# Kernel optimization log

Hardware: AMD Instinct MI355X
Metric: run time of the kernel (lower is better)

The kernel has to match this reference:

```python
import jax, jax.numpy as jnp
import numpy as np

D_MODEL = 1024
NUM_HEADS = 16
HEAD_DIM = D_MODEL // NUM_HEADS


def setup_inputs() -> dict:
    key = jax.random.key(0)
    ks = jax.random.split(key, 7)
    B, S = 2, 2048
    scale = 1.0 / np.sqrt(D_MODEL)
    inp = {
        "input": jax.random.normal(ks[0], (B, S, D_MODEL), dtype=jnp.float32),
        "W_q": jax.random.normal(ks[1], (D_MODEL, D_MODEL), dtype=jnp.float32) * scale,
        "b_q": jax.random.normal(ks[2], (D_MODEL,), dtype=jnp.float32) * 0.01,
        "W_k": jax.random.normal(ks[3], (D_MODEL, D_MODEL), dtype=jnp.float32) * scale,
        "b_k": jax.random.normal(ks[4], (D_MODEL,), dtype=jnp.float32) * 0.01,
        "W_v": jax.random.normal(ks[5], (D_MODEL, D_MODEL), dtype=jnp.float32) * scale,
        "b_v": jax.random.normal(ks[6], (D_MODEL,), dtype=jnp.float32) * 0.01,
    }
    return inp


def reference(input, W_q, b_q, W_k, b_k, W_v, b_v):
    B, S, _ = input.shape
    # QKV projections (torch nn.Linear: x @ W^T + b); split heads -> [B,H,S,Dh]
    def proj(W, b):
        y = jnp.einsum('bsd,ed->bse', input, W) + b
        return y.reshape(B, S, NUM_HEADS, HEAD_DIM).transpose(0, 2, 1, 3)

    Q = proj(W_q, b_q)
    K = proj(W_k, b_k)
    V = proj(W_v, b_v)

    scores = jnp.einsum('bhqd,bhkd->bhqk', Q, K) / jnp.sqrt(
        jnp.asarray(HEAD_DIM, dtype=input.dtype))
    attention_weights = jax.nn.softmax(scores, axis=-1)  # [B,H,S,S]
    out = jnp.einsum('bhqk,bhkd->bhqd', attention_weights, V)
    out = out.transpose(0, 2, 1, 3).reshape(B, S, D_MODEL)
    return out, attention_weights
```

## Files before the change

kernel.cpp:

```cpp
#include <hip/hip_runtime.h>
#include <stdint.h>

#define S_LEN   2048
#define D_MODEL 1024
#define N_HEADS 16
#define HEAD_D  64
#define BATCH   2
#define M_TOT   (BATCH * S_LEN)

typedef __attribute__((ext_vector_type(8))) short s8v;
typedef __attribute__((ext_vector_type(4))) float f4v;
typedef __attribute__((ext_vector_type(4))) unsigned short u4v;

__device__ __forceinline__ float bf2f(unsigned short u) {
    union { unsigned int i; float f; } c; c.i = ((unsigned int)u) << 16; return c.f;
}
__device__ __forceinline__ unsigned short f2bf(float f) {
    union { float f; unsigned int i; } c; c.f = f;
    unsigned int u = c.i + 0x7FFFu + ((c.i >> 16) & 1u);
    return (unsigned short)(u >> 16);
}
__device__ __forceinline__ unsigned int pk2bf(float lo, float hi) {
    return (unsigned int)f2bf(lo) | ((unsigned int)f2bf(hi) << 16);
}
__device__ __forceinline__ float hw_exp2(float x) { return __builtin_amdgcn_exp2f(x); }

#define GLD16(gp, lp) __builtin_amdgcn_global_load_lds(                      \
    (const __attribute__((address_space(1))) void*)(const void*)(gp),        \
    (__attribute__((address_space(3))) void*)(void*)(lp), 16, 0, 0)

#define BAR_LGKM() asm volatile("s_waitcnt lgkmcnt(0)\n\ts_barrier" ::: "memory")

#define EXP_SCALE 0.1803368801111204f

__global__ __launch_bounds__(256) void cvt_bf16(const float* __restrict__ src,
                                                unsigned short* __restrict__ dst, int n) {
    int i = (blockIdx.x * 256 + threadIdx.x) * 4;
    int stride = gridDim.x * 1024;
    for (; i < n; i += stride) {
        float4 v = *(const float4*)(src + i);
        u4v o;
        o[0] = f2bf(v.x); o[1] = f2bf(v.y); o[2] = f2bf(v.z); o[3] = f2bf(v.w);
        *(u4v*)(dst + i) = o;
    }
}

__global__ __launch_bounds__(256) void qkv_gemm(
    const unsigned short* __restrict__ X,
    const unsigned short* __restrict__ Wq, const unsigned short* __restrict__ Wk,
    const unsigned short* __restrict__ Wv,
    const float* __restrict__ bq, const float* __restrict__ bk, const float* __restrict__ bv,
    unsigned short* __restrict__ q_ws, unsigned short* __restrict__ k_ws,
    unsigned short* __restrict__ vt_ws) {
    __shared__ unsigned short sA[128 * 32];
    __shared__ unsigned short sB[128 * 32];

    const int z = blockIdx.z;
    const unsigned short* Wm = (z == 0) ? Wq : ((z == 1) ? Wk : Wv);
    const float* bm = (z == 0) ? bq : ((z == 1) ? bk : bv);
    const int m0 = blockIdx.x * 128, n0 = blockIdx.y * 128;
    const int t = threadIdx.x;
    const int lane = t & 63, w = t >> 6;
    const int fr = lane & 15, g = lane >> 4;
    const int wr = w >> 1, wc = w & 1;

    f4v acc[4][4];
#pragma unroll
    for (int i = 0; i < 4; ++i)
#pragma unroll
        for (int j = 0; j < 4; ++j) acc[i][j] = (f4v){0.f, 0.f, 0.f, 0.f};

    const int rowL = t >> 2;
    const int colL = (t & 3) * 8;
    const unsigned short* gA = X + (size_t)(m0 + rowL) * D_MODEL + colL;
    const unsigned short* gB = Wm + (size_t)(n0 + rowL) * D_MODEL + colL;

    for (int kb = 0; kb < 32; ++kb) {
        const int k0 = kb * 32;
        GLD16(gA + k0,                 sA + w * 512);
        GLD16(gA + 64 * D_MODEL + k0,  sA + 2048 + w * 512);
        GLD16(gB + k0,                 sB + w * 512);
        GLD16(gB + 64 * D_MODEL + k0,  sB + 2048 + w * 512);
        __syncthreads();

        s8v af[4], bfv[4];
#pragma unroll
        for (int i = 0; i < 4; ++i)
            af[i] = *(const s8v*)(sA + (wr * 64 + i * 16 + fr) * 32 + g * 8);
#pragma unroll
        for (int j = 0; j < 4; ++j)
            bfv[j] = *(const s8v*)(sB + (wc * 64 + j * 16 + fr) * 32 + g * 8);
#pragma unroll
        for (int i = 0; i < 4; ++i)
#pragma unroll
            for (int j = 0; j < 4; ++j)
                acc[i][j] = __builtin_amdgcn_mfma_f32_16x16x32_bf16(af[i], bfv[j], acc[i][j], 0, 0, 0);
        __syncthreads();
    }

    const int e_base = n0 + wc * 64;
    const int m_base = m0 + wr * 64;
    if (z < 2) {
        unsigned short* dst = (z == 0) ? q_ws : k_ws;
#pragma unroll
        for (int i = 0; i < 4; ++i) {
#pragma unroll
            for (int j = 0; j < 4; ++j) {
                const int e = e_base + j * 16 + fr;
                const int h = e >> 6, dh = e & 63;
                const float bias = bm[e];
                const int mr = m_base + i * 16 + g * 4;
                const int b_ = mr >> 11, srow = mr & 2047;
                const size_t base = (((size_t)(b_ * N_HEADS + h) * S_LEN + srow) << 6) + dh;
#pragma unroll
                for (int r = 0; r < 4; ++r)
                    dst[base + ((size_t)r << 6)] = f2bf(acc[i][j][r] + bias);
            }
        }
    } else {
#pragma unroll
        for (int i = 0; i < 4; ++i) {
#pragma unroll
            for (int j = 0; j < 4; ++j) {
                const int e = e_base + j * 16 + fr;
                const int h = e >> 6, dh = e & 63;
                const float bias = bm[e];
                const int mr = m_base + i * 16 + g * 4;
                const int b_ = mr >> 11, srow = mr & 2047;
                u4v pk;
#pragma unroll
                for (int r = 0; r < 4; ++r) pk[r] = f2bf(acc[i][j][r] + bias);
                *(u4v*)(vt_ws + ((size_t)(b_ * N_HEADS + h) * HEAD_D + dh) * S_LEN + srow) = pk;
            }
        }
    }
}

__global__ __launch_bounds__(256, 4) void attn_fused6(
    const unsigned short* __restrict__ q_ws, const unsigned short* __restrict__ k_ws,
    const unsigned short* __restrict__ vt_ws,
    float* __restrict__ out, float* __restrict__ wts) {
    __shared__ __align__(16) char SM[40960];

    const int t = threadIdx.x, lane = t & 63, w = t >> 6;
    const int fr = lane & 15, g = lane >> 4;
    const int blk = blockIdx.x;
    const int bh = (blk & 7) * 4 + (blk >> 8);
    const int qt = (blk >> 3) & 31;

    const unsigned short* Qp = q_ws + ((size_t)bh * S_LEN + qt * 64 + w * 16) * HEAD_D;
    const unsigned short* Kp = k_ws + (size_t)bh * S_LEN * HEAD_D;
    const unsigned short* Vt = vt_ws + (size_t)bh * HEAD_D * S_LEN;

    const s8v qa0 = *(const s8v*)(Qp + fr * HEAD_D + g * 8);
    const s8v qa1 = *(const s8v*)(Qp + fr * HEAD_D + 32 + g * 8);

    auto stageK64 = [&](int c, char* dst) {
#pragma unroll
        for (int j = 0; j < 2; ++j) {
            const int d = t * 16 + j * 4096;
            const int row = d >> 7, cb = (d >> 4) & 7;
            GLD16(Kp + (size_t)(c * 64 + row) * HEAD_D + ((cb ^ (row & 7)) << 3),
                  dst + w * 1024 + j * 4096);
        }
    };
    auto stageV64 = [&](int c, char* dst) {
#pragma unroll
        for (int j = 0; j < 2; ++j) {
            const int d = t * 16 + j * 4096;
            const int row = d >> 7, cb = (d >> 4) & 7;
            GLD16(Vt + (size_t)row * S_LEN + c * 64 + ((cb ^ (row & 7)) << 3),
                  dst + w * 1024 + j * 4096);
        }
    };
    auto stageK128 = [&](int c, char* dst) {
#pragma unroll
        for (int j = 0; j < 4; ++j) {
            const int d = t * 16 + j * 4096;
            const int row = d >> 7, cb = (d >> 4) & 7;
            GLD16(Kp + (size_t)(c * 128 + row) * HEAD_D + ((cb ^ (row & 7)) << 3),
                  dst + w * 1024 + j * 4096);
        }
    };
    auto qk16 = [&](const char* kb, int st) -> f4v {
        const int row = st * 16 + fr, m = row & 7;
        const s8v ka0 = *(const s8v*)(kb + row * 128 + ((g ^ m) << 4));
        const s8v ka1 = *(const s8v*)(kb + row * 128 + (((4 + g) ^ m) << 4));
        f4v s = (f4v){0.f, 0.f, 0.f, 0.f};
        s = __builtin_amdgcn_mfma_f32_16x16x32_bf16(ka0, qa0, s, 0, 0, 0);
        s = __builtin_amdgcn_mfma_f32_16x16x32_bf16(ka1, qa1, s, 0, 0, 0);
        return s;
    };

    float rsum = 0.f;
    stageK128(0, SM);
    for (int c = 0; c < 16; ++c) {
        const int cur = c & 1;
        if (c < 15) stageK128(c + 1, SM + (cur ^ 1) * 16384);
        if (c < 15) asm volatile("s_waitcnt vmcnt(4)" ::: "memory");
        else        asm volatile("s_waitcnt vmcnt(0)" ::: "memory");
        asm volatile("s_barrier" ::: "memory");
        const char* kb = SM + cur * 16384;
#pragma unroll
        for (int st = 0; st < 8; ++st) {
            const f4v s = qk16(kb, st);
#pragma unroll
            for (int r = 0; r < 4; ++r) rsum += hw_exp2(s[r] * EXP_SCALE);
        }
        BAR_LGKM();
    }
    rsum += __shfl_xor(rsum, 16);
    rsum += __shfl_xor(rsum, 32);
    const float inv = 1.f / rsum;

    f4v acc[4];
#pragma unroll
    for (int i = 0; i < 4; ++i) acc[i] = (f4v){0.f, 0.f, 0.f, 0.f};
    unsigned short* PL = (unsigned short*)(SM + 32768 + w * 2048);
    const int swp = (fr & 7) << 4;
    float* wbase = wts + ((size_t)bh * S_LEN + qt * 64 + w * 16) * S_LEN;

    stageK64(0, SM); stageV64(0, SM + 16384);
    for (int c = 0; c < 32; ++c) {
        const int cur = c & 1;
        if (c < 31) { stageK64(c + 1, SM + (cur ^ 1) * 8192);
                      stageV64(c + 1, SM + 16384 + (cur ^ 1) * 8192); }
        if (c == 0)      asm volatile("s_waitcnt vmcnt(4)" ::: "memory");
        else if (c < 31) asm volatile("s_waitcnt vmcnt(8)" ::: "memory");
        else             asm volatile("s_waitcnt vmcnt(4)" ::: "memory");
        asm volatile("s_barrier" ::: "memory");

        const char* kb = SM + cur * 8192;
#pragma unroll
        for (int st = 0; st < 4; ++st) {
            const f4v s = qk16(kb, st);
            f4v p;
#pragma unroll
            for (int r = 0; r < 4; ++r) p[r] = hw_exp2(s[r] * EXP_SCALE) * inv;
            const int base = fr * 128 + st * 32 + g * 8;
            *(unsigned int*)((char*)PL + ((base)     ^ swp)) = pk2bf(p[0], p[1]);
            *(unsigned int*)((char*)PL + ((base + 4) ^ swp)) = pk2bf(p[2], p[3]);
        }

        {
            const int r0 = lane >> 4, cc = lane & 15;
#pragma unroll
            for (int i = 0; i < 4; ++i) {
                const int row = i * 4 + r0;
                const u4v pw = *(const u4v*)((const char*)PL +
                                             ((row * 128 + cc * 8) ^ ((row & 7) << 4)));
                f4v o;
#pragma unroll
                for (int e = 0; e < 4; ++e) o[e] = bf2f(pw[e]);
                __builtin_nontemporal_store(o,
                    (f4v*)(wbase + (size_t)row * S_LEN + c * 64 + cc * 4));
            }
        }

        const char* vl = SM + 16384 + cur * 8192;
#pragma unroll
        for (int ks = 0; ks < 2; ++ks) {
            const s8v pa = *(const s8v*)((const char*)PL +
                                         ((fr * 128 + ks * 64 + g * 16) ^ swp));
#pragma unroll
            for (int tt = 0; tt < 4; ++tt) {
                const int vrow = tt * 16 + fr;
                const s8v vv = *(const s8v*)(vl + vrow * 128 +
                                             (((ks * 4 + g) ^ (vrow & 7)) << 4));
                acc[tt] = __builtin_amdgcn_mfma_f32_16x16x32_bf16(pa, vv, acc[tt], 0, 0, 0);
            }
        }
        BAR_LGKM();
    }

    const int b_ = bh >> 4, h = bh & 15;
#pragma unroll
    for (int tt = 0; tt < 4; ++tt)
#pragma unroll
        for (int r = 0; r < 4; ++r)
            __builtin_nontemporal_store(acc[tt][r],
                &out[((size_t)b_ * S_LEN + qt * 64 + w * 16 + g * 4 + r) * D_MODEL +
                     h * HEAD_D + tt * 16 + fr]);
}

extern "C" void kernel_launch(void* const* d_in, const int* in_sizes, int n_in,
                              void* d_out, int out_size, void* d_ws, size_t ws_size,
                              hipStream_t stream) {
    const float* x  = (const float*)d_in[0];
    const float* Wq = (const float*)d_in[1];
    const float* bq = (const float*)d_in[2];
    const float* Wk = (const float*)d_in[3];
    const float* bk = (const float*)d_in[4];
    const float* Wv = (const float*)d_in[5];
    const float* bv = (const float*)d_in[6];

    float* out = (float*)d_out;
    float* wts = out + (size_t)BATCH * S_LEN * D_MODEL;

    unsigned short* xb    = (unsigned short*)d_ws;
    unsigned short* wqb   = xb  + (size_t)M_TOT * D_MODEL;
    unsigned short* wkb   = wqb + (size_t)D_MODEL * D_MODEL;
    unsigned short* wvb   = wkb + (size_t)D_MODEL * D_MODEL;
    unsigned short* q_ws  = wvb + (size_t)D_MODEL * D_MODEL;
    unsigned short* k_ws  = q_ws + (size_t)M_TOT * D_MODEL;
    unsigned short* vt_ws = k_ws + (size_t)M_TOT * D_MODEL;

    cvt_bf16<<<1024, 256, 0, stream>>>(x,  xb,  M_TOT * D_MODEL);
    cvt_bf16<<<256,  256, 0, stream>>>(Wq, wqb, D_MODEL * D_MODEL);
    cvt_bf16<<<256,  256, 0, stream>>>(Wk, wkb, D_MODEL * D_MODEL);
    cvt_bf16<<<256,  256, 0, stream>>>(Wv, wvb, D_MODEL * D_MODEL);

    qkv_gemm<<<dim3(32, 8, 3), 256, 0, stream>>>(xb, wqb, wkb, wvb, bq, bk, bv,
                                                 q_ws, k_ws, vt_ws);

    attn_fused6<<<BATCH * N_HEADS * (S_LEN / 64), 256, 0, stream>>>(q_ws, k_ws, vt_ws, out, wts);
}
```

Measured before the change: 197.9 us.

## Process two query tiles per block, fusing second tile's row-sum into first pass

Each block now handles two 64-row query tiles instead of one, with half as many blocks. The separate row-sum pass for the second tile is folded into the first tile's output pass, reusing the K tiles already staged in shared memory. This cuts total K streaming from three passes per tile to an average of two. The cost is half the grid size and a launch bound of 2 blocks per CU, which may lower occupancy and latency hiding.

```diff
diff --git a/kernel.cpp b/kernel.cpp
--- a/kernel.cpp
+++ b/kernel.cpp
@@ -136,7 +136,7 @@
     }
 }
 
-__global__ __launch_bounds__(256, 4) void attn_fused6(
+__global__ __launch_bounds__(256, 2) void attn_fused7(
     const unsigned short* __restrict__ q_ws, const unsigned short* __restrict__ k_ws,
     const unsigned short* __restrict__ vt_ws,
     float* __restrict__ out, float* __restrict__ wts) {
@@ -145,15 +145,20 @@
     const int t = threadIdx.x, lane = t & 63, w = t >> 6;
     const int fr = lane & 15, g = lane >> 4;
     const int blk = blockIdx.x;
-    const int bh = (blk & 7) * 4 + (blk >> 8);
-    const int qt = (blk >> 3) & 31;
-
-    const unsigned short* Qp = q_ws + ((size_t)bh * S_LEN + qt * 64 + w * 16) * HEAD_D;
+    const int bh = (blk & 7) * 4 + (blk >> 7);
+    const int tp = (blk >> 3) & 15;
+    const int q0 = tp * 128 + w * 16;
+    const int q1 = q0 + 64;
+
     const unsigned short* Kp = k_ws + (size_t)bh * S_LEN * HEAD_D;
     const unsigned short* Vt = vt_ws + (size_t)bh * HEAD_D * S_LEN;
-
-    const s8v qa0 = *(const s8v*)(Qp + fr * HEAD_D + g * 8);
-    const s8v qa1 = *(const s8v*)(Qp + fr * HEAD_D + 32 + g * 8);
+    const unsigned short* Qp0 = q_ws + ((size_t)bh * S_LEN + q0) * HEAD_D;
+    const unsigned short* Qp1 = q_ws + ((size_t)bh * S_LEN + q1) * HEAD_D;
+
+    const s8v qa00 = *(const s8v*)(Qp0 + fr * HEAD_D + g * 8);
+    const s8v qa01 = *(const s8v*)(Qp0 + fr * HEAD_D + 32 + g * 8);
+    const s8v qa10 = *(const s8v*)(Qp1 + fr * HEAD_D + g * 8);
+    const s8v qa11 = *(const s8v*)(Qp1 + fr * HEAD_D + 32 + g * 8);
 
     auto stageK64 = [&](int c, char* dst) {
 #pragma unroll
@@ -182,17 +187,21 @@
                   dst + w * 1024 + j * 4096);
         }
     };
-    auto qk16 = [&](const char* kb, int st) -> f4v {
+    auto qk16 = [&](const char* kb, int st, const s8v& a0, const s8v& a1) -> f4v {
         const int row = st * 16 + fr, m = row & 7;
         const s8v ka0 = *(const s8v*)(kb + row * 128 + ((g ^ m) << 4));
         const s8v ka1 = *(const s8v*)(kb + row * 128 + (((4 + g) ^ m) << 4));
         f4v s = (f4v){0.f, 0.f, 0.f, 0.f};
-        s = __builtin_amdgcn_mfma_f32_16x16x32_bf16(ka0, qa0, s, 0, 0, 0);
-        s = __builtin_amdgcn_mfma_f32_16x16x32_bf16(ka1, qa1, s, 0, 0, 0);
+        s = __builtin_amdgcn_mfma_f32_16x16x32_bf16(ka0, a0, s, 0, 0, 0);
+        s = __builtin_amdgcn_mfma_f32_16x16x32_bf16(ka1, a1, s, 0, 0, 0);
         return s;
     };
 
-    float rsum = 0.f;
+    unsigned short* PL = (unsigned short*)(SM + 32768 + w * 2048);
+    const int swp = (fr & 7) << 4;
+    const int b_ = bh >> 4, h = bh & 15;
+
+    float rsum0 = 0.f;
     stageK128(0, SM);
     for (int c = 0; c < 16; ++c) {
         const int cur = c & 1;
@@ -203,22 +212,21 @@
         const char* kb = SM + cur * 16384;
 #pragma unroll
         for (int st = 0; st < 8; ++st) {
-            const f4v s = qk16(kb, st);
-#pragma unroll
-            for (int r = 0; r < 4; ++r) rsum += hw_exp2(s[r] * EXP_SCALE);
+            const f4v s = qk16(kb, st, qa00, qa01);
+#pragma unroll
+            for (int r = 0; r < 4; ++r) rsum0 += hw_exp2(s[r] * EXP_SCALE);
         }
         BAR_LGKM();
     }
-    rsum += __shfl_xor(rsum, 16);
-    rsum += __shfl_xor(rsum, 32);
-    const float inv = 1.f / rsum;
+    rsum0 += __shfl_xor(rsum0, 16);
+    rsum0 += __shfl_xor(rsum0, 32);
+    const float inv0 = 1.f / rsum0;
 
     f4v acc[4];
 #pragma unroll
     for (int i = 0; i < 4; ++i) acc[i] = (f4v){0.f, 0.f, 0.f, 0.f};
-    unsigned short* PL = (unsigned short*)(SM + 32768 + w * 2048);
-    const int swp = (fr & 7) << 4;
-    float* wbase = wts + ((size_t)bh * S_LEN + qt * 64 + w * 16) * S_LEN;
+    float rsum1 = 0.f;
+    float* wbase0 = wts + ((size_t)bh * S_LEN + q0) * S_LEN;
 
     stageK64(0, SM); stageV64(0, SM + 16384);
     for (int c = 0; c < 32; ++c) {
@@ -233,15 +241,14 @@
         const char* kb = SM + cur * 8192;
 #pragma unroll
         for (int st = 0; st < 4; ++st) {
-            const f4v s = qk16(kb, st);
+            const f4v s = qk16(kb, st, qa00, qa01);
             f4v p;
 #pragma unroll
-            for (int r = 0; r < 4; ++r) p[r] = hw_exp2(s[r] * EXP_SCALE) * inv;
+            for (int r = 0; r < 4; ++r) p[r] = hw_exp2(s[r] * EXP_SCALE) * inv0;
             const int base = fr * 128 + st * 32 + g * 8;
             *(unsigned int*)((char*)PL + ((base)     ^ swp)) = pk2bf(p[0], p[1]);
             *(unsigned int*)((char*)PL + ((base + 4) ^ swp)) = pk2bf(p[2], p[3]);
         }
-
         {
             const int r0 = lane >> 4, cc = lane & 15;
 #pragma unroll
@@ -253,10 +260,15 @@
 #pragma unroll
                 for (int e = 0; e < 4; ++e) o[e] = bf2f(pw[e]);
                 __builtin_nontemporal_store(o,
-                    (f4v*)(wbase + (size_t)row * S_LEN + c * 64 + cc * 4));
-            }
-        }
-
+                    (f4v*)(wbase0 + (size_t)row * S_LEN + c * 64 + cc * 4));
+            }
+        }
+#pragma unroll
+        for (int st = 0; st < 4; ++st) {
+            const f4v s = qk16(kb, st, qa10, qa11);
+#pragma unroll
+            for (int r = 0; r < 4; ++r) rsum1 += hw_exp2(s[r] * EXP_SCALE);
+        }
         const char* vl = SM + 16384 + cur * 8192;
 #pragma unroll
         for (int ks = 0; ks < 2; ++ks) {
@@ -272,14 +284,79 @@
         }
         BAR_LGKM();
     }
-
-    const int b_ = bh >> 4, h = bh & 15;
+    rsum1 += __shfl_xor(rsum1, 16);
+    rsum1 += __shfl_xor(rsum1, 32);
+    const float inv1 = 1.f / rsum1;
+
 #pragma unroll
     for (int tt = 0; tt < 4; ++tt)
 #pragma unroll
         for (int r = 0; r < 4; ++r)
             __builtin_nontemporal_store(acc[tt][r],
-                &out[((size_t)b_ * S_LEN + qt * 64 + w * 16 + g * 4 + r) * D_MODEL +
+                &out[((size_t)b_ * S_LEN + q0 + g * 4 + r) * D_MODEL +
+                     h * HEAD_D + tt * 16 + fr]);
+
+#pragma unroll
+    for (int i = 0; i < 4; ++i) acc[i] = (f4v){0.f, 0.f, 0.f, 0.f};
+    float* wbase1 = wts + ((size_t)bh * S_LEN + q1) * S_LEN;
+
+    stageK64(0, SM); stageV64(0, SM + 16384);
+    for (int c = 0; c < 32; ++c) {
+        const int cur = c & 1;
+        if (c < 31) { stageK64(c + 1, SM + (cur ^ 1) * 8192);
+                      stageV64(c + 1, SM + 16384 + (cur ^ 1) * 8192); }
+        if (c == 0)      asm volatile("s_waitcnt vmcnt(4)" ::: "memory");
+        else if (c < 31) asm volatile("s_waitcnt vmcnt(8)" ::: "memory");
+        else             asm volatile("s_waitcnt vmcnt(4)" ::: "memory");
+        asm volatile("s_barrier" ::: "memory");
+
+        const char* kb = SM + cur * 8192;
+#pragma unroll
+        for (int st = 0; st < 4; ++st) {
+            const f4v s = qk16(kb, st, qa10, qa11);
+            f4v p;
+#pragma unroll
+            for (int r = 0; r < 4; ++r) p[r] = hw_exp2(s[r] * EXP_SCALE) * inv1;
+            const int base = fr * 128 + st * 32 + g * 8;
+            *(unsigned int*)((char*)PL + ((base)     ^ swp)) = pk2bf(p[0], p[1]);
+            *(unsigned int*)((char*)PL + ((base + 4) ^ swp)) = pk2bf(p[2], p[3]);
+        }
+        {
+            const int r0 = lane >> 4, cc = lane & 15;
+#pragma unroll
+            for (int i = 0; i < 4; ++i) {
+                const int row = i * 4 + r0;
+                const u4v pw = *(const u4v*)((const char*)PL +
+                                             ((row * 128 + cc * 8) ^ ((row & 7) << 4)));
+                f4v o;
+#pragma unroll
+                for (int e = 0; e < 4; ++e) o[e] = bf2f(pw[e]);
+                __builtin_nontemporal_store(o,
+                    (f4v*)(wbase1 + (size_t)row * S_LEN + c * 64 + cc * 4));
+            }
+        }
+        const char* vl = SM + 16384 + cur * 8192;
+#pragma unroll
+        for (int ks = 0; ks < 2; ++ks) {
+            const s8v pa = *(const s8v*)((const char*)PL +
+                                         ((fr * 128 + ks * 64 + g * 16) ^ swp));
+#pragma unroll
+            for (int tt = 0; tt < 4; ++tt) {
+                const int vrow = tt * 16 + fr;
+                const s8v vv = *(const s8v*)(vl + vrow * 128 +
+                                             (((ks * 4 + g) ^ (vrow & 7)) << 4));
+                acc[tt] = __builtin_amdgcn_mfma_f32_16x16x32_bf16(pa, vv, acc[tt], 0, 0, 0);
+            }
+        }
+        BAR_LGKM();
+    }
+
+#pragma unroll
+    for (int tt = 0; tt < 4; ++tt)
+#pragma unroll
+        for (int r = 0; r < 4; ++r)
+            __builtin_nontemporal_store(acc[tt][r],
+                &out[((size_t)b_ * S_LEN + q1 + g * 4 + r) * D_MODEL +
                      h * HEAD_D + tt * 16 + fr]);
 }
 
@@ -313,5 +390,5 @@
     qkv_gemm<<<dim3(32, 8, 3), 256, 0, stream>>>(xb, wqb, wkb, wvb, bq, bk, bv,
                                                  q_ws, k_ws, vt_ws);
 
-    attn_fused6<<<BATCH * N_HEADS * (S_LEN / 64), 256, 0, stream>>>(q_ws, k_ws, vt_ws, out, wts);
-}
+    attn_fused7<<<512, 256, 0, stream>>>(q_ws, k_ws, vt_ws, out, wts);
+}
```

Measured after the change: 192.4 us. -2.8%, faster.
